# Kernel optimization log

Measured on AMD Instinct MI355X. Metric: run time of the kernel, lower is better.

## Reference

```python
import jax, jax.numpy as jnp
import numpy as np

D_MODEL = 2048
NUM_GROUPS = 16
D_HEAD = D_MODEL // NUM_GROUPS
ROTARY_DIM = int(D_MODEL * 0.25)  # 512


def setup_inputs() -> dict:
    key = jax.random.key(0)
    ks = jax.random.split(key, 8)
    B, S, N = 4, 2048, 2048
    scale = 1.0 / np.sqrt(D_MODEL)
    return {
        "query": jax.random.normal(ks[0], (B, S, D_MODEL), jnp.float32),
        "key": jax.random.normal(ks[1], (B, N, D_MODEL), jnp.float32),
        "value": jax.random.normal(ks[2], (B, N, D_MODEL), jnp.float32),
        "mask": jax.random.randint(ks[3], (B, S), 0, 2, jnp.int32),
        "position_ids": jnp.arange(S, dtype=jnp.int64) if jax.config.jax_enable_x64 else jnp.arange(S, dtype=jnp.int32),
        "Wq": jax.random.normal(ks[4], (D_MODEL, D_MODEL), jnp.float32) * scale,
        "Wk": jax.random.normal(ks[5], (D_MODEL, D_MODEL), jnp.float32) * scale,
        "Wv": jax.random.normal(ks[6], (D_MODEL, D_MODEL), jnp.float32) * scale,
        "Wo": jax.random.normal(ks[7], (D_MODEL, D_MODEL), jnp.float32) * scale,
    }


def _apply_rope_query_only(q, k, position_ids):
    # Faithful to source: rotary embedding is applied to query ONLY; key is returned unchanged.
    rd = ROTARY_DIM
    pos = position_ids.astype(q.dtype)  # (S,)
    freq = jnp.arange(0, rd, 2, dtype=q.dtype)
    inv_freq = 1.0 / (10000.0 ** (freq / rd))  # (rd/2,)
    pe = pos[:, None] * inv_freq[None, :]       # (S, rd/2)
    cos = jnp.tile(jnp.cos(pe), (1, 2))[None]   # (1, S, rd) tiled [c, c]
    sin = jnp.tile(jnp.sin(pe), (1, 2))[None]
    q_rot, q_pass = q[..., :rd], q[..., rd:]
    half = rd // 2
    q_rot_half = jnp.concatenate([-q_rot[..., half:], q_rot[..., :half]], axis=-1)
    q_rot = q_rot * cos + q_rot_half * sin
    q = jnp.concatenate([q_rot, q_pass], axis=-1)
    return q, k


def reference(query, key, value, mask, position_ids, Wq, Wk, Wv, Wo):
    B, S, _ = query.shape
    N = key.shape[1]
    G, dh = NUM_GROUPS, D_HEAD

    q = query @ Wq.T
    k = key @ Wk.T
    v = value @ Wv.T

    q, k = _apply_rope_query_only(q, k, position_ids)

    qh = q.reshape(B, S, G, dh).transpose(0, 2, 1, 3)  # (B,G,S,dh)
    kh = k.reshape(B, N, G, dh).transpose(0, 2, 1, 3)  # (B,G,N,dh)
    vh = v.reshape(B, N, G, dh).transpose(0, 2, 1, 3)  # (B,G,N,dh)

    scores = jnp.einsum("bgsd,bgnd->bgsn", qh, kh) / jnp.sqrt(jnp.asarray(dh, q.dtype))
    # mask (B,S) -> (B,1,1,N); here S == N so pad width is 0 (pad value 1 in source)
    m = mask[:, None, None, :]
    scores = jnp.where(m == 0, -jnp.inf, scores)

    w = jax.nn.softmax(scores, axis=-1)
    out = jnp.einsum("bgsn,bgnd->bgsd", w, vh)           # (B,G,S,dh)
    out = out.transpose(0, 2, 1, 3).reshape(B, S, D_MODEL)
    return out @ Wo.T
```

## Files before the change

kernel.cpp:

```cpp
#include <hip/hip_runtime.h>
#include <hip/hip_bf16.h>
#include <type_traits>
#include <utility>

typedef unsigned short u16;
typedef unsigned int u32;
typedef __attribute__((ext_vector_type(8))) short  s16x8;
typedef __attribute__((ext_vector_type(4))) short  s16x4;
typedef __attribute__((ext_vector_type(4))) float  f32x4;
typedef __attribute__((ext_vector_type(16))) float f32x16;
typedef __bf16 bf16x8_t __attribute__((ext_vector_type(8)));
typedef __bf16 bf16x2_t __attribute__((ext_vector_type(2)));

#define SEQ 2048
#define DMODEL 2048
#define NBATCH 4
#define DH 128
#define NB (NBATCH * SEQ)

#define QK_SCALE_LOG2 0.12754375f
#define BIAS_VALID  (-34.624681f)
#define BIAS_MASKED (-180.0f)

#if __has_builtin(__builtin_amdgcn_exp2f)
#define EXP2(x) __builtin_amdgcn_exp2f(x)
#else
#define EXP2(x) exp2f(x)
#endif

#define BARRIER __builtin_amdgcn_s_barrier()
#define FENCE  asm volatile("" ::: "memory")
#define LGKM0  asm volatile("s_waitcnt lgkmcnt(0)" ::: "memory")
#define VMCNT4 asm volatile("s_waitcnt vmcnt(4)" ::: "memory")
#define VMCNT0 asm volatile("s_waitcnt vmcnt(0)" ::: "memory")

static __device__ __forceinline__ u16 f2bf(float f) {
  unsigned u = __float_as_uint(f);
  u += 0x7fffu + ((u >> 16) & 1u);
  return (u16)(u >> 16);
}
static __device__ __forceinline__ float bf2f(u16 h) {
  return __uint_as_float(((unsigned)h) << 16);
}
static __device__ __forceinline__ u32 pack_bf16(float a, float b) {
  bf16x2_t t; t[0] = (__bf16)a; t[1] = (__bf16)b;
  return __builtin_bit_cast(u32, t);
}
static __device__ __forceinline__ void plswap(u32& a, u32& b) {
  asm("v_permlane32_swap_b32 %0, %1" : "+v"(a), "+v"(b));
}

template <typename T, typename = void>
struct mfma_takes : std::false_type {};
template <typename T>
struct mfma_takes<T, std::void_t<decltype(__builtin_amdgcn_mfma_f32_16x16x32_bf16(
    std::declval<T>(), std::declval<T>(), std::declval<f32x4>(), 0, 0, 0))>>
    : std::true_type {};
using mfma_frag_t = std::conditional_t<mfma_takes<s16x8>::value, s16x8, bf16x8_t>;

static __device__ __forceinline__ f32x16 mfma32(s16x8 a, s16x8 b, f32x16 c) {
  return __builtin_amdgcn_mfma_f32_32x32x16_bf16(
      __builtin_bit_cast(mfma_frag_t, a), __builtin_bit_cast(mfma_frag_t, b), c, 0, 0, 0);
}

typedef const void __attribute__((address_space(1)))* gas_ptr;
typedef void __attribute__((address_space(3)))* las_ptr;
static __device__ __forceinline__ void gload16(const void* g, void* l) {
  __builtin_amdgcn_global_load_lds((gas_ptr)g, (las_ptr)l, 16, 0, 0);
}

static __device__ __forceinline__ s16x8 frag_from_words(u32 w0, u32 w1, u32 w2, u32 w3) {
  union { u32 w[4]; s16x8 v; } u;
  u.w[0] = w0; u.w[1] = w1; u.w[2] = w2; u.w[3] = w3;
  return u.v;
}

static __device__ __forceinline__ void cvt8(const float* src, u16* dst, int i) {
  const float4* p = (const float4*)src + (size_t)i * 2;
  float4 a = p[0], b4 = p[1];
  s16x8 o;
  o[0] = (short)f2bf(a.x);  o[1] = (short)f2bf(a.y);
  o[2] = (short)f2bf(a.z);  o[3] = (short)f2bf(a.w);
  o[4] = (short)f2bf(b4.x); o[5] = (short)f2bf(b4.y);
  o[6] = (short)f2bf(b4.z); o[7] = (short)f2bf(b4.w);
  *(s16x8*)(dst + (size_t)i * 8) = o;
}

__global__ void cvt3_k(const float* __restrict__ a, const float* __restrict__ b,
                       const float* __restrict__ c, u16* __restrict__ oa,
                       u16* __restrict__ ob, u16* __restrict__ oc) {
  const int n8 = 1 << 21;
  const int stride = (int)(gridDim.x * blockDim.x);
  for (int i = (int)(blockIdx.x * blockDim.x + threadIdx.x); i < 3 * n8; i += stride) {
    const int seg = i >> 21, off = i & (n8 - 1);
    const float* src = seg == 0 ? a : (seg == 1 ? b : c);
    u16* dst = seg == 0 ? oa : (seg == 1 ? ob : oc);
    cvt8(src, dst, off);
  }
}

__global__ void cvt4_k(const float* __restrict__ a, const float* __restrict__ b,
                       const float* __restrict__ c, const float* __restrict__ d,
                       u16* __restrict__ oa, u16* __restrict__ ob,
                       u16* __restrict__ oc, u16* __restrict__ od) {
  const int n8 = 1 << 19;
  const int stride = (int)(gridDim.x * blockDim.x);
  for (int i = (int)(blockIdx.x * blockDim.x + threadIdx.x); i < 4 * n8; i += stride) {
    const int seg = i >> 19, off = i & (n8 - 1);
    const float* src = seg == 0 ? a : (seg == 1 ? b : (seg == 2 ? c : d));
    u16* dst = seg == 0 ? oa : (seg == 1 ? ob : (seg == 2 ? oc : od));
    cvt8(src, dst, off);
  }
}

__global__ void bias_k(const int* __restrict__ mask, u16* __restrict__ biasv, int n) {
  const int i = (int)(blockIdx.x * blockDim.x + threadIdx.x);
  if (i < n) biasv[i] = mask[i] ? f2bf(BIAS_VALID) : f2bf(BIAS_MASKED);
}

template <int OUT_MODE>
__global__ __launch_bounds__(512, 2) void gemm256_k(const u16* __restrict__ A,
                                                    const u16* __restrict__ Bw,
                                                    void* __restrict__ Cv) {
  constexpr int M = 8192, N = 2048, K = 2048;
  constexpr int NT = K / 64;
  __shared__ u16 Ab[2][256 * 64];
  __shared__ u16 Bb[2][256 * 64];

  const int tid = (int)threadIdx.x;
  const int wv = tid >> 6, lane = tid & 63;
  const int l32 = lane & 31, hi = lane >> 5;
  const int wm = wv >> 2, wn = wv & 3;

  const int bid = (int)blockIdx.x;
  const int bn = (bid >> 3) & 7;
  const int bm = (bid & 7) * 4 + (bid >> 6);

  const size_t arow0 = (size_t)bm * 256;
  const size_t brow0 = (size_t)bn * 256;

  const int srow = tid >> 3;
  const int scolb = (tid & 7) * 16;
  const int scol = (scolb ^ ((srow & 7) << 4)) >> 1;
  const u16* agp = A  + (arow0 + srow) * (size_t)K + scol;
  const u16* bgp = Bw + (brow0 + srow) * (size_t)K + scol;

  f32x16 acc[4][2];
#pragma unroll
  for (int mi = 0; mi < 4; ++mi)
#pragma unroll
    for (int ni = 0; ni < 2; ++ni)
#pragma unroll
      for (int r = 0; r < 16; ++r) acc[mi][ni][r] = 0.f;

  auto SH_A = [&](int kt2, u16* bufA, int half) {
#pragma unroll
    for (int j = 0; j < 2; ++j) {
      const int rb = half * 128 + j * 64;
      gload16(agp + (size_t)rb * K + kt2, bufA + (rb + wv * 8) * 64);
    }
  };
  auto SH_B = [&](int kt2, u16* bufB, int half) {
#pragma unroll
    for (int j = 0; j < 2; ++j) {
      const int rb = half * 128 + j * 64;
      gload16(bgp + (size_t)rb * K + kt2, bufB + (rb + wv * 8) * 64);
    }
  };
  auto LDA = [&](const u16* buf, int qm, s16x8* af) {
#pragma unroll
    for (int mb = 0; mb < 2; ++mb) {
      const int row = wm * 128 + qm * 64 + mb * 32 + l32;
#pragma unroll
      for (int ks = 0; ks < 4; ++ks) {
        const int cb = ((ks * 32 + hi * 16) ^ ((row & 7) << 4)) >> 1;
        af[mb * 4 + ks] = *(const s16x8*)&buf[row * 64 + cb];
      }
    }
  };
  auto LDB = [&](const u16* buf, int qn, s16x8* bfr) {
    const int row = wn * 64 + qn * 32 + l32;
#pragma unroll
    for (int ks = 0; ks < 4; ++ks) {
      const int cb = ((ks * 32 + hi * 16) ^ ((row & 7) << 4)) >> 1;
      bfr[ks] = *(const s16x8*)&buf[row * 64 + cb];
    }
  };
  auto MM = [&](const s16x8* af, const s16x8* bfr, int qm, int qn) {
    __builtin_amdgcn_s_setprio(1);
#pragma unroll
    for (int mb = 0; mb < 2; ++mb)
#pragma unroll
      for (int ks = 0; ks < 4; ++ks)
        acc[qm * 2 + mb][qn] = mfma32(af[mb * 4 + ks], bfr[ks], acc[qm * 2 + mb][qn]);
    __builtin_amdgcn_s_setprio(0);
  };

  SH_A(0, Ab[0], 0); SH_A(0, Ab[0], 1);
  SH_B(0, Bb[0], 0); SH_B(0, Bb[0], 1);
  SH_B(64, Bb[1], 0); SH_B(64, Bb[1], 1);
  VMCNT4; BARRIER;

  for (int t = 0; t < NT; ++t) {
    u16* Ac = Ab[t & 1];
    u16* Bc = Bb[t & 1];
    u16* An = Ab[(t + 1) & 1];
    u16* Bn = Bb[t & 1];
    const int kA = (t + 1) * 64;
    const int kB = (t + 2) * 64;
    const bool stA = (t + 1 < NT);
    const bool stB = (t + 2 < NT);
    s16x8 af0[8], af1[8], bf0[4], bf1[4];

    LDA(Ac, 0, af0); LDB(Bc, 0, bf0);
    if (stA) SH_A(kA, An, 0);
    BARRIER; LGKM0;
    MM(af0, bf0, 0, 0);
    BARRIER;
    LDB(Bc, 1, bf1);
    if (stA) SH_A(kA, An, 1);
    BARRIER; LGKM0;
    MM(af0, bf1, 0, 1);
    BARRIER;
    LDA(Ac, 1, af1);
    if (stB) SH_B(kB, Bn, 0);
    BARRIER; LGKM0;
    MM(af1, bf1, 1, 1);
    BARRIER;
    if (stB) { SH_B(kB, Bn, 1); VMCNT4; }
    else if (stA) { VMCNT0; }
    BARRIER; LGKM0;
    MM(af1, bf0, 1, 0);
    BARRIER;
  }

  const size_t row0 = arow0 + (size_t)wm * 128;
  const size_t col0 = brow0 + (size_t)wn * 64;
#pragma unroll
  for (int mi = 0; mi < 4; ++mi)
#pragma unroll
    for (int ni = 0; ni < 2; ++ni) {
      const size_t rbase = row0 + mi * 32 + 4 * hi;
      const size_t c = col0 + ni * 32 + l32;
      if constexpr (OUT_MODE == 0) {
        u16* C = (u16*)Cv;
#pragma unroll
        for (int q = 0; q < 4; ++q)
#pragma unroll
          for (int rr = 0; rr < 4; ++rr)
            C[(rbase + 8 * q + rr) * N + c] = f2bf(acc[mi][ni][q * 4 + rr]);
      } else if constexpr (OUT_MODE == 1) {
        float* C = (float*)Cv;
#pragma unroll
        for (int q = 0; q < 4; ++q)
#pragma unroll
          for (int rr = 0; rr < 4; ++rr)
            C[(rbase + 8 * q + rr) * N + c] = acc[mi][ni][q * 4 + rr];
      } else {
        u16* C = (u16*)Cv;
#pragma unroll
        for (int q = 0; q < 4; ++q) {
          s16x4 v;
#pragma unroll
          for (int rr = 0; rr < 4; ++rr) v[rr] = (short)f2bf(acc[mi][ni][q * 4 + rr]);
          *(s16x4*)&C[c * (size_t)M + rbase + 8 * q] = v;
        }
      }
    }
}

__global__ void rope_k(u16* __restrict__ qb, const int* __restrict__ pos_ids) {
  const int row = (int)blockIdx.x;
  const int s = row & (SEQ - 1);
  const int t = (int)threadIdx.x;
  const float pos = (float)pos_ids[s];
  const float ang = pos * exp2f((float)t * (-13.287712379549449f / 256.0f));
  float sn, cs;
  sincosf(ang, &sn, &cs);
  u16* p = qb + (size_t)row * DMODEL;
  const float x = bf2f(p[t]);
  const float y = bf2f(p[t + 256]);
  p[t]       = f2bf((x * cs - y * sn) * QK_SCALE_LOG2);
  p[t + 256] = f2bf((y * cs + x * sn) * QK_SCALE_LOG2);
#pragma unroll
  for (int j = 0; j < 6; ++j) {
    const int d = 512 + t + 256 * j;
    p[d] = f2bf(bf2f(p[d]) * QK_SCALE_LOG2);
  }
}

__device__ __forceinline__ void attn_stage(u16* Ks, u16* Vs,
                                           const u16* kbase, const u16* vbase,
                                           int kt, int w, int lane) {
#pragma unroll
  for (int i = 0; i < 4; ++i) {
    const int row = w * 16 + i * 4 + (lane >> 4);
    const int srcb = ((lane & 15) * 16) ^ ((row & 7) << 4);
    gload16(kbase + (size_t)(kt + row) * DMODEL + (srcb >> 1), &Ks[(w * 16 + i * 4) * 128]);
  }
#pragma unroll
  for (int i = 0; i < 4; ++i) {
    const int row = w * 32 + i * 8 + (lane >> 3);
    const int srcb = ((lane & 7) * 16) ^ ((row & 7) << 4);
    gload16(vbase + (size_t)row * NB + kt + (srcb >> 1), &Vs[(w * 32 + i * 8) * 64]);
  }
}

__global__ __launch_bounds__(256) void attn_k(const u16* __restrict__ q,
                                              const u16* __restrict__ k,
                                              const u16* __restrict__ vt,
                                              const u16* __restrict__ biasv,
                                              u16* __restrict__ att) {
  __shared__ u16 Ks[2][64 * 128];
  __shared__ u16 Vs[2][128 * 64];

  const int tid = (int)threadIdx.x;
  const int w = tid >> 6, lane = tid & 63;
  const int l32 = lane & 31, hi = lane >> 5;

  const int bid = (int)blockIdx.x;
  const int sb = (bid & 7) * 128 + (bid >> 3);
  const int qt = sb & 15;
  const int bg = sb >> 4;
  const int b = bg >> 4, g = bg & 15;

  const int qrow = qt * 128 + w * 32 + l32;
  const u16* qp = q + ((size_t)b * SEQ + qrow) * DMODEL + g * DH;
  s16x8 aq[8];
#pragma unroll
  for (int s = 0; s < 8; ++s) aq[s] = *(const s16x8*)(qp + s * 16 + hi * 8);

  const u32 one0 = (hi == 0) ? 0x00003F80u : 0u;
  const s16x8 bones = frag_from_words(one0, 0, 0, 0);
  const s16x8 allones = frag_from_words(0x3F803F80u, 0x3F803F80u, 0x3F803F80u, 0x3F803F80u);

  f32x16 oacc[4], lacc;
#pragma unroll
  for (int r = 0; r < 16; ++r) {
    lacc[r] = 0.f;
#pragma unroll
    for (int d0 = 0; d0 < 4; ++d0) oacc[d0][r] = 0.f;
  }

  const u16* kbase = k + (size_t)b * SEQ * DMODEL + g * DH;
  const u16* vbase = vt + (size_t)(g * DH) * NB + (size_t)b * SEQ;
  const u16* bbase = biasv + b * SEQ;

  attn_stage(Ks[0], Vs[0], kbase, vbase, 0, w, lane);
  u16 bb0 = bbase[l32], bb1 = bbase[32 + l32];

  for (int t = 0; t < 32; ++t) {
    const int cur = t & 1;
    __syncthreads();
    u16 bbn0 = bb0, bbn1 = bb1;
    if (t < 31) {
      attn_stage(Ks[cur ^ 1], Vs[cur ^ 1], kbase, vbase, (t + 1) * 64, w, lane);
      bbn0 = bbase[(t + 1) * 64 + l32];
      bbn1 = bbase[(t + 1) * 64 + 32 + l32];
    }
    const u16* KsC = Ks[cur];
    const u16* VsC = Vs[cur];

    const s16x8 ab0 = frag_from_words((hi == 0) ? (u32)bb0 : 0u, 0, 0, 0);
    const s16x8 ab1 = frag_from_words((hi == 0) ? (u32)bb1 : 0u, 0, 0, 0);
    __builtin_amdgcn_s_setprio(1);
    f32x16 sacc0 = mfma32(ab0, bones, (f32x16)(0.f));
    f32x16 sacc1 = mfma32(ab1, bones, (f32x16)(0.f));

#pragma unroll
    for (int s = 0; s < 8; ++s) {
      const int byteoff = ((s * 32 + hi * 16) ^ ((l32 & 7) << 4)) >> 1;
      const s16x8 a0 = *(const s16x8*)&KsC[l32 * 128 + byteoff];
      const s16x8 a1 = *(const s16x8*)&KsC[(32 + l32) * 128 + byteoff];
      sacc0 = mfma32(a0, aq[s], sacc0);
      sacc1 = mfma32(a1, aq[s], sacc1);
    }
    __builtin_amdgcn_s_setprio(0);

    u32 pk0[8], pk1[8];
#pragma unroll
    for (int i = 0; i < 8; ++i) {
      pk0[i] = pack_bf16(EXP2(sacc0[2 * i]), EXP2(sacc0[2 * i + 1]));
      pk1[i] = pack_bf16(EXP2(sacc1[2 * i]), EXP2(sacc1[2 * i + 1]));
    }
    s16x8 pa[4];
#pragma unroll
    for (int grp = 0; grp < 4; ++grp) {
      u32* pk = (grp < 2) ? pk0 : pk1;
      const int o = (grp & 1) * 4;
      plswap(pk[o + 0], pk[o + 2]);
      plswap(pk[o + 1], pk[o + 3]);
      pa[grp] = frag_from_words(pk[o + 0], pk[o + 1], pk[o + 2], pk[o + 3]);
    }

    __builtin_amdgcn_s_setprio(1);
#pragma unroll
    for (int ks = 0; ks < 4; ++ks) lacc = mfma32(pa[ks], allones, lacc);

#pragma unroll
    for (int d0 = 0; d0 < 4; ++d0) {
      const int rowd = d0 * 32 + l32;
#pragma unroll
      for (int ks = 0; ks < 4; ++ks) {
        const int byteoff = ((ks * 32 + hi * 16) ^ ((rowd & 7) << 4)) >> 1;
        const s16x8 bv = *(const s16x8*)&VsC[rowd * 64 + byteoff];
        oacc[d0] = mfma32(pa[ks], bv, oacc[d0]);
      }
    }
    __builtin_amdgcn_s_setprio(0);
    bb0 = bbn0; bb1 = bbn1;
  }

  float rinv[16];
#pragma unroll
  for (int r = 0; r < 16; ++r) rinv[r] = 1.0f / lacc[r];
  u16* ob = att + ((size_t)b * SEQ + qt * 128 + w * 32) * DMODEL + g * DH;
#pragma unroll
  for (int d0 = 0; d0 < 4; ++d0)
#pragma unroll
    for (int r = 0; r < 16; ++r) {
      const int qloc = (r & 3) + 8 * (r >> 2) + 4 * hi;
      ob[(size_t)qloc * DMODEL + d0 * 32 + l32] = f2bf(oacc[d0][r] * rinv[r]);
    }
}

extern "C" void kernel_launch(void* const* d_in, const int* in_sizes, int n_in,
                              void* d_out, int out_size, void* d_ws, size_t ws_size,
                              hipStream_t stream) {
  const float* query = (const float*)d_in[0];
  const float* key   = (const float*)d_in[1];
  const float* value = (const float*)d_in[2];
  const int*   maskp = (const int*)d_in[3];
  const int*   posp  = (const int*)d_in[4];
  const float* Wq    = (const float*)d_in[5];
  const float* Wk    = (const float*)d_in[6];
  const float* Wv    = (const float*)d_in[7];
  const float* Wo    = (const float*)d_in[8];

  char* ws = (char*)d_ws;
  const size_t MB = 1024ull * 1024ull;
  u16* wq_b = (u16*)(ws + 0 * MB);
  u16* wk_b = (u16*)(ws + 8 * MB);
  u16* wv_b = (u16*)(ws + 16 * MB);
  u16* wo_b = (u16*)(ws + 24 * MB);
  u16* xq   = (u16*)(ws + 32 * MB);
  u16* xk   = (u16*)(ws + 64 * MB);
  u16* xv   = (u16*)(ws + 96 * MB);
  u16* qb   = (u16*)(ws + 128 * MB);
  u16* kb   = (u16*)(ws + 160 * MB);
  u16* vtb  = (u16*)(ws + 192 * MB);
  u16* att  = xq;
  u16* biasv = xk;

  cvt3_k<<<dim3(2048), dim3(256), 0, stream>>>(query, key, value, xq, xk, xv);
  cvt4_k<<<dim3(1024), dim3(256), 0, stream>>>(Wq, Wk, Wv, Wo, wq_b, wk_b, wv_b, wo_b);

  gemm256_k<0><<<dim3(256), dim3(512), 0, stream>>>(xq, wq_b, (void*)qb);
  gemm256_k<0><<<dim3(256), dim3(512), 0, stream>>>(xk, wk_b, (void*)kb);
  gemm256_k<2><<<dim3(256), dim3(512), 0, stream>>>(xv, wv_b, (void*)vtb);

  bias_k<<<dim3((NBATCH * SEQ + 255) / 256), dim3(256), 0, stream>>>(maskp, biasv, NBATCH * SEQ);

  rope_k<<<dim3(NBATCH * SEQ), dim3(256), 0, stream>>>(qb, posp);

  attn_k<<<dim3(1024), dim3(256), 0, stream>>>(qb, kb, vtb, biasv, att);

  gemm256_k<1><<<dim3(256), dim3(512), 0, stream>>>(att, wo_b, d_out);

  (void)in_sizes; (void)n_in; (void)out_size; (void)ws_size;
}
```

Baseline: 599.2 us.

## Compact unmasked keys/values before projection and attention to skip masked work

Scans the mask per batch to build a compacted index of valid key positions, then gathers and converts only those key/value rows to bf16. The K/V projection GEMMs run only over the compacted rows, and attention iterates only over the tiles that hold valid keys. The three projection GEMMs are also merged into one launch with a runtime output mode. This is meant to roughly halve K/V projection and attention work under the random mask. The cost is a serial single-block scan, a gather with indirect row access, and runtime instead of compile-time output-mode branches in the GEMM.

```diff
diff --git a/kernel.cpp b/kernel.cpp
--- a/kernel.cpp
+++ b/kernel.cpp
@@ -86,17 +86,10 @@
   *(s16x8*)(dst + (size_t)i * 8) = o;
 }
 
-__global__ void cvt3_k(const float* __restrict__ a, const float* __restrict__ b,
-                       const float* __restrict__ c, u16* __restrict__ oa,
-                       u16* __restrict__ ob, u16* __restrict__ oc) {
-  const int n8 = 1 << 21;
+__global__ void cvt1_k(const float* __restrict__ in, u16* __restrict__ out, int n8) {
   const int stride = (int)(gridDim.x * blockDim.x);
-  for (int i = (int)(blockIdx.x * blockDim.x + threadIdx.x); i < 3 * n8; i += stride) {
-    const int seg = i >> 21, off = i & (n8 - 1);
-    const float* src = seg == 0 ? a : (seg == 1 ? b : c);
-    u16* dst = seg == 0 ? oa : (seg == 1 ? ob : oc);
-    cvt8(src, dst, off);
-  }
+  for (int i = (int)(blockIdx.x * blockDim.x + threadIdx.x); i < n8; i += stride)
+    cvt8(in, out, i);
 }
 
 __global__ void cvt4_k(const float* __restrict__ a, const float* __restrict__ b,
@@ -113,15 +106,61 @@
   }
 }
 
-__global__ void bias_k(const int* __restrict__ mask, u16* __restrict__ biasv, int n) {
-  const int i = (int)(blockIdx.x * blockDim.x + threadIdx.x);
-  if (i < n) biasv[i] = mask[i] ? f2bf(BIAS_VALID) : f2bf(BIAS_MASKED);
-}
-
-template <int OUT_MODE>
-__global__ __launch_bounds__(512, 2) void gemm256_k(const u16* __restrict__ A,
-                                                    const u16* __restrict__ Bw,
-                                                    void* __restrict__ Cv) {
+__global__ void scan_k(const int* __restrict__ mask, int* __restrict__ idx,
+                       u16* __restrict__ biasc, int* __restrict__ meta) {
+  __shared__ int nv_sh[4];
+  const int tid = (int)threadIdx.x;
+  const int w = tid >> 6, lane = tid & 63;
+  const int* mb = mask + w * SEQ;
+  int cnt = 0;
+  for (int it = 0; it < SEQ / 64; ++it) {
+    const int i = it * 64 + lane;
+    const bool m = mb[i] != 0;
+    const unsigned long long bal = __ballot(m);
+    const int pos = cnt + __popcll(bal & ((1ull << lane) - 1ull));
+    if (m) idx[w * SEQ + pos] = i;
+    cnt += __popcll(bal);
+  }
+  if (lane == 0) nv_sh[w] = cnt;
+  __syncthreads();
+  const int nv = nv_sh[w];
+  const int npad = (nv + 255) & ~255;
+  for (int j = nv + lane; j < npad; j += 64) idx[w * SEQ + j] = 0;
+  for (int j = lane; j < SEQ; j += 64)
+    biasc[w * SEQ + j] = (j < nv) ? f2bf(BIAS_VALID) : f2bf(BIAS_MASKED);
+  if (tid == 0) {
+    int off = 0;
+    for (int b2 = 0; b2 < 4; ++b2) {
+      const int nvb = nv_sh[b2];
+      meta[b2] = off;
+      meta[4 + b2] = (nvb + 63) >> 6;
+      off += (nvb + 255) & ~255;
+    }
+    meta[8] = off;
+  }
+}
+
+__global__ void gathercvt_k(const float* __restrict__ keyf,
+                            const float* __restrict__ valf,
+                            const int* __restrict__ idx, const int* __restrict__ meta,
+                            u16* __restrict__ xkc, u16* __restrict__ xvc) {
+  const int b = (int)blockIdx.y;
+  const int j = (int)blockIdx.x;
+  const int mstart = meta[b];
+  const int mend = (b < 3) ? meta[b + 1] : meta[8];
+  if (mstart + j >= mend) return;
+  const int src = idx[b * SEQ + j];
+  const float* ks = keyf + ((size_t)b * SEQ + src) * DMODEL;
+  const float* vs = valf + ((size_t)b * SEQ + src) * DMODEL;
+  u16* kd = xkc + (size_t)(mstart + j) * DMODEL;
+  u16* vd = xvc + (size_t)(mstart + j) * DMODEL;
+  cvt8(ks, kd, (int)threadIdx.x);
+  cvt8(vs, vd, (int)threadIdx.x);
+}
+
+static __device__ void gemm_body(const u16* __restrict__ A, const u16* __restrict__ Bw,
+                                 void* __restrict__ Cv, const int outmode,
+                                 const int bid, const int mlimit) {
   constexpr int M = 8192, N = 2048, K = 2048;
   constexpr int NT = K / 64;
   __shared__ u16 Ab[2][256 * 64];
@@ -132,9 +171,9 @@
   const int l32 = lane & 31, hi = lane >> 5;
   const int wm = wv >> 2, wn = wv & 3;
 
-  const int bid = (int)blockIdx.x;
   const int bn = (bid >> 3) & 7;
   const int bm = (bid & 7) * 4 + (bid >> 6);
+  if (bm * 256 >= mlimit) return;
 
   const size_t arow0 = (size_t)bm * 256;
   const size_t brow0 = (size_t)bn * 256;
@@ -242,14 +281,14 @@
     for (int ni = 0; ni < 2; ++ni) {
       const size_t rbase = row0 + mi * 32 + 4 * hi;
       const size_t c = col0 + ni * 32 + l32;
-      if constexpr (OUT_MODE == 0) {
+      if (outmode == 0) {
         u16* C = (u16*)Cv;
 #pragma unroll
         for (int q = 0; q < 4; ++q)
 #pragma unroll
           for (int rr = 0; rr < 4; ++rr)
             C[(rbase + 8 * q + rr) * N + c] = f2bf(acc[mi][ni][q * 4 + rr]);
-      } else if constexpr (OUT_MODE == 1) {
+      } else if (outmode == 1) {
         float* C = (float*)Cv;
 #pragma unroll
         for (int q = 0; q < 4; ++q)
@@ -267,6 +306,24 @@
         }
       }
     }
+}
+
+__global__ __launch_bounds__(512, 2) void gemmproj_k(
+    const u16* __restrict__ xq, const u16* __restrict__ wq, u16* __restrict__ qout,
+    const u16* __restrict__ xkc, const u16* __restrict__ wk, u16* __restrict__ kout,
+    const u16* __restrict__ xvc, const u16* __restrict__ wv, u16* __restrict__ vtout,
+    const int* __restrict__ meta) {
+  const int seg = (int)blockIdx.x >> 8;
+  const int bid = (int)blockIdx.x & 255;
+  if (seg == 0)      gemm_body(xq, wq, (void*)qout, 0, bid, 8192);
+  else if (seg == 1) gemm_body(xkc, wk, (void*)kout, 0, bid, meta[8]);
+  else               gemm_body(xvc, wv, (void*)vtout, 2, bid, meta[8]);
+}
+
+__global__ __launch_bounds__(512, 2) void gemmwo_k(const u16* __restrict__ A,
+                                                   const u16* __restrict__ Bw,
+                                                   float* __restrict__ C) {
+  gemm_body(A, Bw, (void*)C, 1, (int)blockIdx.x, 8192);
 }
 
 __global__ void rope_k(u16* __restrict__ qb, const int* __restrict__ pos_ids) {
@@ -307,9 +364,10 @@
 }
 
 __global__ __launch_bounds__(256) void attn_k(const u16* __restrict__ q,
-                                              const u16* __restrict__ k,
-                                              const u16* __restrict__ vt,
-                                              const u16* __restrict__ biasv,
+                                              const u16* __restrict__ kc,
+                                              const u16* __restrict__ vtc,
+                                              const u16* __restrict__ biasc,
+                                              const int* __restrict__ meta,
                                               u16* __restrict__ att) {
   __shared__ u16 Ks[2][64 * 128];
   __shared__ u16 Vs[2][128 * 64];
@@ -324,6 +382,9 @@
   const int bg = sb >> 4;
   const int b = bg >> 4, g = bg & 15;
 
+  const int mstart = meta[b];
+  const int nt = meta[4 + b];
+
   const int qrow = qt * 128 + w * 32 + l32;
   const u16* qp = q + ((size_t)b * SEQ + qrow) * DMODEL + g * DH;
   s16x8 aq[8];
@@ -342,18 +403,18 @@
     for (int d0 = 0; d0 < 4; ++d0) oacc[d0][r] = 0.f;
   }
 
-  const u16* kbase = k + (size_t)b * SEQ * DMODEL + g * DH;
-  const u16* vbase = vt + (size_t)(g * DH) * NB + (size_t)b * SEQ;
-  const u16* bbase = biasv + b * SEQ;
+  const u16* kbase = kc + (size_t)mstart * DMODEL + g * DH;
+  const u16* vbase = vtc + (size_t)(g * DH) * NB + mstart;
+  const u16* bbase = biasc + b * SEQ;
 
   attn_stage(Ks[0], Vs[0], kbase, vbase, 0, w, lane);
   u16 bb0 = bbase[l32], bb1 = bbase[32 + l32];
 
-  for (int t = 0; t < 32; ++t) {
+  for (int t = 0; t < nt; ++t) {
     const int cur = t & 1;
     __syncthreads();
     u16 bbn0 = bb0, bbn1 = bb1;
-    if (t < 31) {
+    if (t < nt - 1) {
       attn_stage(Ks[cur ^ 1], Vs[cur ^ 1], kbase, vbase, (t + 1) * 64, w, lane);
       bbn0 = bbase[(t + 1) * 64 + l32];
       bbn1 = bbase[(t + 1) * 64 + 32 + l32];
@@ -444,28 +505,30 @@
   u16* wv_b = (u16*)(ws + 16 * MB);
   u16* wo_b = (u16*)(ws + 24 * MB);
   u16* xq   = (u16*)(ws + 32 * MB);
-  u16* xk   = (u16*)(ws + 64 * MB);
-  u16* xv   = (u16*)(ws + 96 * MB);
+  u16* xkc  = (u16*)(ws + 64 * MB);
+  u16* xvc  = (u16*)(ws + 96 * MB);
   u16* qb   = (u16*)(ws + 128 * MB);
-  u16* kb   = (u16*)(ws + 160 * MB);
-  u16* vtb  = (u16*)(ws + 192 * MB);
-  u16* att  = xq;
-  u16* biasv = xk;
-
-  cvt3_k<<<dim3(2048), dim3(256), 0, stream>>>(query, key, value, xq, xk, xv);
+  u16* kc   = (u16*)(ws + 160 * MB);
+  u16* vtc  = (u16*)(ws + 192 * MB);
+  char* aux = ws + 224 * MB;
+  int* meta  = (int*)aux;
+  int* idx   = (int*)(aux + 256);
+  u16* biasc = (u16*)(aux + 256 + 32768);
+  u16* att   = xq;
+
+  scan_k<<<dim3(1), dim3(256), 0, stream>>>(maskp, idx, biasc, meta);
+  cvt1_k<<<dim3(2048), dim3(256), 0, stream>>>(query, xq, (NBATCH * SEQ * DMODEL) / 8);
+  gathercvt_k<<<dim3(SEQ, NBATCH), dim3(256), 0, stream>>>(key, value, idx, meta, xkc, xvc);
   cvt4_k<<<dim3(1024), dim3(256), 0, stream>>>(Wq, Wk, Wv, Wo, wq_b, wk_b, wv_b, wo_b);
 
-  gemm256_k<0><<<dim3(256), dim3(512), 0, stream>>>(xq, wq_b, (void*)qb);
-  gemm256_k<0><<<dim3(256), dim3(512), 0, stream>>>(xk, wk_b, (void*)kb);
-  gemm256_k<2><<<dim3(256), dim3(512), 0, stream>>>(xv, wv_b, (void*)vtb);
-
-  bias_k<<<dim3((NBATCH * SEQ + 255) / 256), dim3(256), 0, stream>>>(maskp, biasv, NBATCH * SEQ);
+  gemmproj_k<<<dim3(768), dim3(512), 0, stream>>>(xq, wq_b, qb, xkc, wk_b, kc,
+                                                  xvc, wv_b, vtc, meta);
 
   rope_k<<<dim3(NBATCH * SEQ), dim3(256), 0, stream>>>(qb, posp);
 
-  attn_k<<<dim3(1024), dim3(256), 0, stream>>>(qb, kb, vtb, biasv, att);
-
-  gemm256_k<1><<<dim3(256), dim3(512), 0, stream>>>(att, wo_b, d_out);
+  attn_k<<<dim3(1024), dim3(256), 0, stream>>>(qb, kc, vtc, biasc, meta, att);
+
+  gemmwo_k<<<dim3(256), dim3(512), 0, stream>>>(att, wo_b, (float*)d_out);
 
   (void)in_sizes; (void)n_in; (void)out_size; (void)ws_size;
 }
```

Measured after the change: 529.4 us. 1.13x faster.
